# Kernel optimization log

Measured on AMD Instinct MI355X. Metric: run time of the kernel, lower is better.

The kernel has to match this reference:

```python
import jax, jax.numpy as jnp
import numpy as np

S = 3072       # packed sequence length
DIM = 1280     # hidden dim
H = 16         # num heads
HD = DIM // H  # head dim = 80
NEG = -1e9     # additive mask value for cross-segment entries


def setup_inputs() -> dict:
    key = jax.random.key(0)
    ks = jax.random.split(key, 6)
    x = jax.random.normal(ks[0], (S, DIM), jnp.float32)
    # rope angle table [S, HD//2]
    rotary_pos_emb = jax.random.uniform(ks[1], (S, HD // 2), jnp.float32, 0.0, 2.0 * np.pi)
    # 4 equal image segments packed together
    cu_seqlens = jnp.array([0, 768, 1536, 2304, 3072], jnp.int32)
    w_qkv = jax.random.normal(ks[2], (3 * DIM, DIM), jnp.float32) * 0.02
    b_qkv = jax.random.normal(ks[3], (3 * DIM,), jnp.float32) * 0.02
    w_proj = jax.random.normal(ks[4], (DIM, DIM), jnp.float32) * 0.02
    b_proj = jax.random.normal(ks[5], (DIM,), jnp.float32) * 0.02
    return {"x": x, "cu_seqlens": cu_seqlens, "rotary_pos_emb": rotary_pos_emb,
            "w_qkv": w_qkv, "b_qkv": b_qkv, "w_proj": w_proj, "b_proj": b_proj}


def _rope(t, cos, sin):
    # t: [S, H, HD]; cos/sin: [S, 1, HD]
    t1, t2 = jnp.split(t, 2, axis=-1)
    rot = jnp.concatenate([-t2, t1], axis=-1)
    return t * cos + rot * sin


def reference(x, cu_seqlens, rotary_pos_emb, w_qkv, b_qkv, w_proj, b_proj):
    s, d = x.shape
    qkv = (x @ w_qkv.T + b_qkv).reshape(s, 3, H, HD)
    q, k, v = qkv[:, 0], qkv[:, 1], qkv[:, 2]  # each [S, H, HD]

    # NeoX-style rope with tiled (repeated) freqs, computed in fp32
    cos = jnp.cos(rotary_pos_emb)
    sin = jnp.sin(rotary_pos_emb)
    cos = jnp.concatenate([cos, cos], axis=-1)[:, None, :]  # [S,1,HD]
    sin = jnp.concatenate([sin, sin], axis=-1)[:, None, :]
    q = _rope(q.astype(jnp.float32), cos, sin).astype(x.dtype)
    k = _rope(k.astype(jnp.float32), cos, sin).astype(x.dtype)

    # block-diagonal varlen mask from cu_seqlens: segment id per position
    seg = jnp.searchsorted(cu_seqlens, jnp.arange(s), side='right') - 1  # [S]
    mask = jnp.where(seg[:, None] == seg[None, :], 0.0, NEG).astype(x.dtype)  # [S,S]

    scale = 1.0 / np.sqrt(HD).astype(np.float32)
    scores = jnp.einsum('qhd,khd->hqk', q, k) * scale + mask[None]  # [H,S,S]
    attn = jax.nn.softmax(scores, axis=-1)
    out = jnp.einsum('hqk,khd->qhd', attn, v).reshape(s, d)  # [S, DIM]
    return out @ w_proj.T + b_proj
```

## Files before the change

kernel.cpp:

```cpp
#include <hip/hip_runtime.h>


typedef __bf16 bf16;
typedef __bf16 bf16x4 __attribute__((ext_vector_type(4)));
typedef __bf16 bf16x8 __attribute__((ext_vector_type(8)));
typedef float f32x4 __attribute__((ext_vector_type(4)));

constexpr int S = 3072;
constexpr int DIM = 1280;
constexpr int H = 16;
constexpr int HD = 80;
constexpr int DP = 96;
constexpr int NQKV = 3 * DIM;

constexpr float QSCALE = 1.4426950408889634f / 8.94427190999916f;

__device__ __forceinline__ void gload_lds16(const void* g, void* l) {
  __builtin_amdgcn_global_load_lds(
      (const __attribute__((address_space(1))) void*)g,
      (__attribute__((address_space(3))) void*)l, 16, 0, 0);
}

constexpr long CN1 = (long)S * DIM;
constexpr long CN2 = (long)NQKV * DIM;

__global__ __launch_bounds__(256) void cvt3(
    const float* __restrict__ x, const float* __restrict__ wq,
    const float* __restrict__ wp, bf16* __restrict__ xo,
    bf16* __restrict__ wqo, bf16* __restrict__ wpo) {
  long i = ((long)blockIdx.x * 256 + threadIdx.x) * 4;
  const float* s;
  bf16* d;
  if (i < CN1) { s = x + i; d = xo + i; }
  else if (i < CN1 + CN2) { s = wq + (i - CN1); d = wqo + (i - CN1); }
  else { s = wp + (i - CN1 - CN2); d = wpo + (i - CN1 - CN2); }
  float4 v = *(const float4*)s;
  bf16x4 o = {(bf16)v.x, (bf16)v.y, (bf16)v.z, (bf16)v.w};
  *(bf16x4*)d = o;
}

template <bool OUT_BF16>
__global__ __launch_bounds__(512, 2) void gemm256(
    const bf16* __restrict__ A, const bf16* __restrict__ B,
    const float* __restrict__ bias, void* __restrict__ Cout, int M, int N,
    int K) {
  extern __shared__ char lds[];
  const int tid = threadIdx.x;
  const int w = tid >> 6, lane = tid & 63;
  const int r15 = lane & 15, b4 = lane >> 4;
  const int wr = w >> 2, wc = w & 3;
  const int nwg = gridDim.x * gridDim.y;
  const int orig = blockIdx.y * gridDim.x + blockIdx.x;
  const int xcd = orig % 8, loc = orig / 8;
  const int qq = nwg / 8, rq = nwg % 8;
  const int swzid =
      (xcd < rq ? xcd * (qq + 1) : rq * (qq + 1) + (xcd - rq) * qq) + loc;
  const int n0 = (swzid % gridDim.x) * 256, m0 = (swzid / gridDim.x) * 256;
  int aRow[2], aCol[2];
#pragma unroll
  for (int i = 0; i < 2; i++) {
    int lin = (w * 2 + i) * 1024 + lane * 16;
    int logi = lin ^ (((lin >> 7) & 7) << 4);
    aRow[i] = logi >> 6;
    aCol[i] = (logi & 63) >> 1;
  }
  const int NT = K / 32;
  auto stage = [&](int kt) {
    char* sa = lds + (kt & 3) * 32768;
    char* sb = sa + 16384;
    const int kb = kt * 32;
#pragma unroll
    for (int i = 0; i < 2; i++) {
      const int lin = (w * 2 + i) * 1024 + lane * 16;
      gload_lds16(A + (size_t)(m0 + aRow[i]) * K + kb + aCol[i], sa + lin);
      gload_lds16(B + (size_t)(n0 + aRow[i]) * K + kb + aCol[i], sb + lin);
    }
  };
  f32x4 acc[8][4] = {};
  stage(0); stage(1); stage(2);
  asm volatile("s_waitcnt vmcnt(8)" ::: "memory");
  __builtin_amdgcn_s_barrier();
  for (int kt = 0; kt < NT; ++kt) {
    const char* As = lds + (kt & 3) * 32768;
    const char* Bs = As + 16384;
    if (kt + 3 < NT) stage(kt + 3);
    bf16x8 af[8], bfr[4];
#pragma unroll
    for (int i = 0; i < 8; i++) {
      int a = (wr * 128 + i * 16 + r15) * 64 + b4 * 16;
      a ^= ((a >> 7) & 7) << 4;
      af[i] = *(const bf16x8*)(As + a);
    }
#pragma unroll
    for (int j = 0; j < 4; j++) {
      int a = (wc * 64 + j * 16 + r15) * 64 + b4 * 16;
      a ^= ((a >> 7) & 7) << 4;
      bfr[j] = *(const bf16x8*)(Bs + a);
    }
    __builtin_amdgcn_s_setprio(1);
#pragma unroll
    for (int i = 0; i < 8; i++)
#pragma unroll
      for (int j = 0; j < 4; j++)
        acc[i][j] = __builtin_amdgcn_mfma_f32_16x16x32_bf16(af[i], bfr[j],
                                                            acc[i][j], 0, 0, 0);
    __builtin_amdgcn_s_setprio(0);
    const int rem = NT - 2 - kt;
    if (rem >= 2)      asm volatile("s_waitcnt vmcnt(8)" ::: "memory");
    else if (rem == 1) asm volatile("s_waitcnt vmcnt(4)" ::: "memory");
    else if (rem == 0) asm volatile("s_waitcnt vmcnt(0)" ::: "memory");
    else               asm volatile("" ::: "memory");
    __builtin_amdgcn_s_barrier();
  }
#pragma unroll
  for (int j = 0; j < 4; j++) {
    const int n = n0 + wc * 64 + j * 16 + r15;
    const float bv = bias[n];
#pragma unroll
    for (int i = 0; i < 8; i++) {
      const int mr = m0 + wr * 128 + i * 16 + b4 * 4;
#pragma unroll
      for (int r = 0; r < 4; r++) {
        float v = acc[i][j][r] + bv;
        if (OUT_BF16)
          ((bf16*)Cout)[(size_t)(mr + r) * N + n] = (bf16)v;
        else
          ((float*)Cout)[(size_t)(mr + r) * N + n] = v;
      }
    }
  }
}

template <bool OUT_BF16>
__global__ __launch_bounds__(256) void gemm_bt(
    const bf16* __restrict__ A, const bf16* __restrict__ B,
    const float* __restrict__ bias, void* __restrict__ Cout, int M, int N,
    int K) {
  __shared__ bf16 Al[2][128 * 32];
  __shared__ bf16 Bl[2][128 * 32];
  const int tid = threadIdx.x;
  const int w = tid >> 6, lane = tid & 63;
  const int r15 = lane & 15, b4 = lane >> 4;
  const int nwg = gridDim.x * gridDim.y;
  const int orig = blockIdx.y * gridDim.x + blockIdx.x;
  const int swzid = (orig & 7) * (nwg >> 3) + (orig >> 3);
  const int bx = swzid % gridDim.x, by = swzid / gridDim.x;
  const int m0 = by * 128, n0 = bx * 128;
  const int wm = (w >> 1) * 64, wn = (w & 1) * 64;
  f32x4 acc[4][4] = {};
  const int row0 = tid >> 2, ko0 = (tid & 3) * 8;
  const bf16* Ar0 = A + (size_t)(m0 + row0) * K + ko0;
  const bf16* Ar1 = A + (size_t)(m0 + row0 + 64) * K + ko0;
  const bf16* Br0 = B + (size_t)(n0 + row0) * K + ko0;
  const bf16* Br1 = B + (size_t)(n0 + row0 + 64) * K + ko0;

  auto stage = [&](int buf, int k0) {
    char* la = (char*)Al[buf] + w * 1024;
    char* lb = (char*)Bl[buf] + w * 1024;
    gload_lds16(Ar0 + k0, la);
    gload_lds16(Ar1 + k0, la + 4096);
    gload_lds16(Br0 + k0, lb);
    gload_lds16(Br1 + k0, lb + 4096);
  };

  stage(0, 0);
  int cur = 0;
  for (int k0 = 0; k0 < K; k0 += 32) {
    __syncthreads();
    if (k0 + 32 < K) stage(cur ^ 1, k0 + 32);
    bf16x8 af[4], bfr[4];
#pragma unroll
    for (int i = 0; i < 4; i++) {
      af[i] = *(const bf16x8*)((const char*)Al[cur] + (wm + i * 16 + r15) * 64 + b4 * 16);
      bfr[i] = *(const bf16x8*)((const char*)Bl[cur] + (wn + i * 16 + r15) * 64 + b4 * 16);
    }
#pragma unroll
    for (int i = 0; i < 4; i++)
#pragma unroll
      for (int j = 0; j < 4; j++)
        acc[i][j] = __builtin_amdgcn_mfma_f32_16x16x32_bf16(af[i], bfr[j], acc[i][j], 0, 0, 0);
    cur ^= 1;
  }
#pragma unroll
  for (int j = 0; j < 4; j++) {
    const int n = n0 + wn + j * 16 + r15;
    const float bv = bias[n];
#pragma unroll
    for (int i = 0; i < 4; i++) {
      const int mr = m0 + wm + i * 16 + b4 * 4;
#pragma unroll
      for (int r = 0; r < 4; r++) {
        float v = acc[i][j][r] + bv;
        if (OUT_BF16)
          ((bf16*)Cout)[(size_t)(mr + r) * N + n] = (bf16)v;
        else
          ((float*)Cout)[(size_t)(mr + r) * N + n] = v;
      }
    }
  }
}

__global__ __launch_bounds__(256) void rope_scatter(
    const bf16* __restrict__ qkv, const float* __restrict__ rp,
    bf16* __restrict__ Qo, bf16* __restrict__ Ko, bf16* __restrict__ VTo) {
  __shared__ bf16 vl[80][72];
  const int h = blockIdx.x / 48, st = blockIdx.x % 48;
  const int tid = threadIdx.x;
#pragma unroll
  for (int c = 0; c < 3; c++) {
    int ch = c * 256 + tid;
    if (ch < 640) {
      int row = ch / 10, ck = ch % 10;
      int s = st * 64 + row;
      bf16x8 v = *(const bf16x8*)(qkv + (size_t)s * NQKV + 2 * DIM + h * HD + ck * 8);
#pragma unroll
      for (int e = 0; e < 8; e++) vl[ck * 8 + e][row] = v[e];
    }
  }
#pragma unroll
  for (int c = 0; c < 3; c++) {
    int ch = c * 256 + tid;
    if (ch < 640) {
      int row = ch / 10, t10 = ch % 10;
      int which = t10 >= 5 ? 1 : 0, cp = t10 % 5;
      int s = st * 64 + row;
      const bf16* src = qkv + (size_t)s * NQKV + which * DIM + h * HD;
      bf16x8 lo = *(const bf16x8*)(src + cp * 8);
      bf16x8 hi = *(const bf16x8*)(src + 40 + cp * 8);
      const float* rr = rp + (size_t)s * 40 + cp * 8;
      float4 a0 = *(const float4*)rr;
      float4 a1 = *(const float4*)(rr + 4);
      float ang[8] = {a0.x, a0.y, a0.z, a0.w, a1.x, a1.y, a1.z, a1.w};
      const float sc = which ? 1.0f : QSCALE;
      bf16x8 olo, ohi;
#pragma unroll
      for (int e = 0; e < 8; e++) {
        float sn, cs;
        __sincosf(ang[e], &sn, &cs);
        float t1 = (float)lo[e], t2 = (float)hi[e];
        olo[e] = (bf16)((t1 * cs - t2 * sn) * sc);
        ohi[e] = (bf16)((t2 * cs + t1 * sn) * sc);
      }
      bf16* dst = (which ? Ko : Qo) + ((size_t)h * S + s) * DP;
      *(bf16x8*)(dst + cp * 8) = olo;
      *(bf16x8*)(dst + 40 + cp * 8) = ohi;
    }
  }
  {
    int row = tid >> 2, slot = tid & 3;
    int s = st * 64 + row;
    bf16* dst = ((slot >> 1) ? Ko : Qo) + ((size_t)h * S + s) * DP + 80 + (slot & 1) * 8;
    bf16x8 z = {};
    *(bf16x8*)dst = z;
  }
  __syncthreads();
#pragma unroll
  for (int c = 0; c < 3; c++) {
    int ch = c * 256 + tid;
    if (ch < 640) {
      int d = ch >> 3, slot = ch & 7;
      *(bf16x8*)(VTo + (size_t)(h * HD + d) * S + st * 64 + slot * 8) =
          *(const bf16x8*)(&vl[d][slot * 8]);
    }
  }
}

__global__ __launch_bounds__(256) void attn_kern(
    const bf16* __restrict__ Qg, const bf16* __restrict__ Kg,
    const bf16* __restrict__ Vg, const int* __restrict__ cu, int nseg,
    bf16* __restrict__ Out) {
  __shared__ bf16 Kl[2][64 * 128];
  __shared__ bf16 Vl[2][80 * 64];
  __shared__ bf16 Pl[4][16 * 64];
  const int tid = threadIdx.x, w = tid >> 6, lane = tid & 63;
  const int r15 = lane & 15, b4 = lane >> 4;
  const int nwg = gridDim.x;
  const int orig = blockIdx.x;
  const int swzb = (orig & 7) * (nwg >> 3) + (orig >> 3);
  const int h = swzb / 48, qt = swzb % 48;
  const int q = qt * 64 + w * 16 + r15;
  int sq = 0, eq = S, lo = 0, hi = S;
  {
    const int qlo = qt * 64, qhi = qt * 64 + 63;
#pragma unroll
    for (int i = 0; i < 8; i++) {
      if (i >= nseg) break;
      int a = cu[i], b = cu[i + 1];
      if (q >= a && q < b) { sq = a; eq = b; }
      if (qlo >= a && qlo < b) lo = a;
      if (qhi >= a && qhi < b) hi = b;
    }
  }
  const int swz = (r15 & 7) << 4;
  bf16x8 qf[3];
  {
    const bf16* qrow = Qg + ((size_t)h * S + q) * DP + b4 * 8;
#pragma unroll
    for (int c = 0; c < 3; c++) qf[c] = *(const bf16x8*)(qrow + c * 32);
  }
  f32x4 o[5] = {};
  float m = -1e30f, l = 0.f;
  const bf16* Kbase = Kg + (size_t)h * S * DP;
  const bf16* Vbase = Vg + (size_t)h * HD * S;

  int krow[3], kslot[3], vd[3], vslot[3];
#pragma unroll
  for (int c = 0; c < 3; c++) {
    int ch = c * 256 + tid;
    krow[c] = ch / 12; kslot[c] = ch % 12;
    vd[c] = ch >> 3;   vslot[c] = ch & 7;
  }
  bf16x8 kreg[3], vreg[3];

  auto load_stage = [&](int k0) {
#pragma unroll
    for (int c = 0; c < 3; c++)
      kreg[c] = *(const bf16x8*)(Kbase + (size_t)(k0 + krow[c]) * DP + kslot[c] * 8);
#pragma unroll
    for (int c = 0; c < 3; c++)
      if (c < 2 || tid < 128)
        vreg[c] = *(const bf16x8*)(Vbase + (size_t)vd[c] * S + k0 + vslot[c] * 8);
  };
  auto write_stage = [&](int buf) {
#pragma unroll
    for (int c = 0; c < 3; c++)
      *(bf16x8*)((char*)Kl[buf] +
                 ((krow[c] * 256 + kslot[c] * 16) ^ ((krow[c] & 7) << 4))) = kreg[c];
#pragma unroll
    for (int c = 0; c < 3; c++)
      if (c < 2 || tid < 128)
        *(bf16x8*)((char*)Vl[buf] +
                   ((vd[c] * 128 + vslot[c] * 16) ^ ((vd[c] & 7) << 4))) = vreg[c];
  };

  const int k0start = lo & ~63;
  load_stage(k0start);
  write_stage(0);
  __syncthreads();
  int cur = 0;
  for (int k0 = k0start; k0 < hi; k0 += 64) {
    const bool more = (k0 + 64 < hi);
    if (more) load_stage(k0 + 64);
    f32x4 st[4] = {};
    __builtin_amdgcn_s_setprio(1);
#pragma unroll
    for (int g = 0; g < 4; g++)
#pragma unroll
      for (int c = 0; c < 3; c++) {
        bf16x8 kf = *(const bf16x8*)((const char*)Kl[cur] +
                                     (((g * 16 + r15) * 256 + c * 64 + b4 * 16) ^ swz));
        st[g] = __builtin_amdgcn_mfma_f32_16x16x32_bf16(kf, qf[c], st[g], 0, 0, 0);
      }
    __builtin_amdgcn_s_setprio(0);
    float sv[16];
    float tm = -3e38f;
    if (k0 >= sq && k0 + 63 < eq) {
#pragma unroll
      for (int g = 0; g < 4; g++)
#pragma unroll
        for (int r = 0; r < 4; r++) {
          sv[g * 4 + r] = st[g][r];
          tm = fmaxf(tm, st[g][r]);
        }
    } else {
#pragma unroll
      for (int g = 0; g < 4; g++)
#pragma unroll
        for (int r = 0; r < 4; r++) {
          int key = k0 + g * 16 + b4 * 4 + r;
          float sc = (key >= sq && key < eq) ? st[g][r] : -1e30f;
          sv[g * 4 + r] = sc;
          tm = fmaxf(tm, sc);
        }
    }
    tm = fmaxf(tm, __shfl_xor(tm, 16));
    tm = fmaxf(tm, __shfl_xor(tm, 32));
    if (!__all(tm <= m + 8.f)) {
      const float mn = fmaxf(m, tm);
      const float alpha = __builtin_amdgcn_exp2f(m - mn);
#pragma unroll
      for (int dg = 0; dg < 5; dg++) o[dg] *= alpha;
      l *= alpha;
      m = mn;
    }
    float rs = 0.f;
#pragma unroll
    for (int g = 0; g < 4; g++) {
      bf16x4 pp;
#pragma unroll
      for (int r = 0; r < 4; r++) {
        float p = __builtin_amdgcn_exp2f(sv[g * 4 + r] - m);
        rs += p;
        pp[r] = (bf16)p;
      }
      *(bf16x4*)((char*)Pl[w] + ((r15 * 128 + g * 32 + b4 * 8) ^ swz)) = pp;
    }
    rs += __shfl_xor(rs, 16);
    rs += __shfl_xor(rs, 32);
    l += rs;
    __builtin_amdgcn_s_setprio(1);
#pragma unroll
    for (int dg = 0; dg < 5; dg++)
#pragma unroll
      for (int c = 0; c < 2; c++) {
        bf16x8 vf = *(const bf16x8*)((const char*)Vl[cur] +
                                     (((dg * 16 + r15) * 128 + c * 64 + b4 * 16) ^ swz));
        bf16x8 pf = *(const bf16x8*)((const char*)Pl[w] +
                                     ((r15 * 128 + c * 64 + b4 * 16) ^ swz));
        o[dg] = __builtin_amdgcn_mfma_f32_16x16x32_bf16(vf, pf, o[dg], 0, 0, 0);
      }
    __builtin_amdgcn_s_setprio(0);
    if (more) write_stage(cur ^ 1);
    __syncthreads();
    cur ^= 1;
  }
  const float inv = 1.f / l;
  bf16* orow = Out + (size_t)q * DIM + h * HD + b4 * 4;
#pragma unroll
  for (int dg = 0; dg < 5; dg++) {
    bf16x4 ov = {(bf16)(o[dg][0] * inv), (bf16)(o[dg][1] * inv),
                 (bf16)(o[dg][2] * inv), (bf16)(o[dg][3] * inv)};
    *(bf16x4*)(orow + dg * 16) = ov;
  }
}

extern "C" void kernel_launch(void* const* d_in, const int* in_sizes, int n_in,
                              void* d_out, int out_size, void* d_ws,
                              size_t ws_size, hipStream_t stream) {
  const float* x = (const float*)d_in[0];
  const int* cu = (const int*)d_in[1];
  const float* rope = (const float*)d_in[2];
  const float* w_qkv = (const float*)d_in[3];
  const float* b_qkv = (const float*)d_in[4];
  const float* w_proj = (const float*)d_in[5];
  const float* b_proj = (const float*)d_in[6];
  const int nseg = in_sizes[1] - 1;

  bf16* x16 = (bf16*)d_ws;
  bf16* wq16 = x16 + (size_t)S * DIM;
  bf16* wp16 = wq16 + (size_t)NQKV * DIM;
  bf16* qkv16 = wp16 + (size_t)DIM * DIM;
  bf16* Qb = qkv16 + (size_t)S * NQKV;
  bf16* Kb = Qb + (size_t)H * S * DP;
  bf16* VTb = Kb + (size_t)H * S * DP;
  bf16* attn16 = VTb + (size_t)H * HD * S;

  cvt3<<<10240, 256, 0, stream>>>(x, w_qkv, w_proj, x16, wq16, wp16);
  gemm256<true><<<dim3(NQKV / 256, S / 256), 512, 131072, stream>>>(
      x16, wq16, b_qkv, qkv16, S, NQKV, DIM);
  rope_scatter<<<H * 48, 256, 0, stream>>>(qkv16, rope, Qb, Kb, VTb);
  attn_kern<<<H * 48, 256, 0, stream>>>(Qb, Kb, VTb, cu, nseg, attn16);
  gemm_bt<false><<<dim3(DIM / 128, S / 128), 256, 0, stream>>>(
      attn16, wp16, b_proj, d_out, S, DIM, DIM);
}
```

Baseline: 132.5 us.

## Split GEMM k-step into two half-phases interleaving A/B prefetch with MFMA

```diff
diff --git a/kernel.cpp b/kernel.cpp
--- a/kernel.cpp
+++ b/kernel.cpp
@@ -56,40 +56,43 @@
   const int swzid =
       (xcd < rq ? xcd * (qq + 1) : rq * (qq + 1) + (xcd - rq) * qq) + loc;
   const int n0 = (swzid % gridDim.x) * 256, m0 = (swzid / gridDim.x) * 256;
-  int aRow[2], aCol[2];
+  const bf16* aSrc[2];
+  const bf16* bSrc[2];
+  int linv[2];
 #pragma unroll
   for (int i = 0; i < 2; i++) {
-    int lin = (w * 2 + i) * 1024 + lane * 16;
-    int logi = lin ^ (((lin >> 7) & 7) << 4);
-    aRow[i] = logi >> 6;
-    aCol[i] = (logi & 63) >> 1;
+    const int lin = tid * 16 + i * 8192;
+    linv[i] = lin;
+    const int logi = lin ^ (((lin >> 7) & 7) << 4);
+    const int row = logi >> 6, col = (logi & 63) >> 1;
+    aSrc[i] = A + (size_t)(m0 + row) * K + col;
+    bSrc[i] = B + (size_t)(n0 + row) * K + col;
   }
   const int NT = K / 32;
-  auto stage = [&](int kt) {
-    char* sa = lds + (kt & 3) * 32768;
-    char* sb = sa + 16384;
-    const int kb = kt * 32;
-#pragma unroll
-    for (int i = 0; i < 2; i++) {
-      const int lin = (w * 2 + i) * 1024 + lane * 16;
-      gload_lds16(A + (size_t)(m0 + aRow[i]) * K + kb + aCol[i], sa + lin);
-      gload_lds16(B + (size_t)(n0 + aRow[i]) * K + kb + aCol[i], sb + lin);
-    }
+  auto stageA = [&](int kt) {
+    char* s = lds + (kt & 3) * 32768;
+#pragma unroll
+    for (int i = 0; i < 2; i++) gload_lds16(aSrc[i] + kt * 32, s + linv[i]);
+  };
+  auto stageB = [&](int kt) {
+    char* s = lds + (kt & 3) * 32768 + 16384;
+#pragma unroll
+    for (int i = 0; i < 2; i++) gload_lds16(bSrc[i] + kt * 32, s + linv[i]);
   };
   f32x4 acc[8][4] = {};
-  stage(0); stage(1); stage(2);
+  stageA(0); stageB(0); stageA(1); stageB(1); stageA(2); stageB(2);
   asm volatile("s_waitcnt vmcnt(8)" ::: "memory");
   __builtin_amdgcn_s_barrier();
   for (int kt = 0; kt < NT; ++kt) {
     const char* As = lds + (kt & 3) * 32768;
     const char* Bs = As + 16384;
-    if (kt + 3 < NT) stage(kt + 3);
-    bf16x8 af[8], bfr[4];
-#pragma unroll
-    for (int i = 0; i < 8; i++) {
+    const bool pf = (kt + 3 < NT);
+    bf16x8 afr[4], bfr[4];
+#pragma unroll
+    for (int i = 0; i < 4; i++) {
       int a = (wr * 128 + i * 16 + r15) * 64 + b4 * 16;
       a ^= ((a >> 7) & 7) << 4;
-      af[i] = *(const bf16x8*)(As + a);
+      afr[i] = *(const bf16x8*)(As + a);
     }
 #pragma unroll
     for (int j = 0; j < 4; j++) {
@@ -97,13 +100,35 @@
       a ^= ((a >> 7) & 7) << 4;
       bfr[j] = *(const bf16x8*)(Bs + a);
     }
+    if (pf) stageA(kt + 3);
+    asm volatile("" ::: "memory");
+    __builtin_amdgcn_s_barrier();
     __builtin_amdgcn_s_setprio(1);
 #pragma unroll
-    for (int i = 0; i < 8; i++)
+    for (int i = 0; i < 4; i++)
 #pragma unroll
       for (int j = 0; j < 4; j++)
-        acc[i][j] = __builtin_amdgcn_mfma_f32_16x16x32_bf16(af[i], bfr[j],
+        acc[i][j] = __builtin_amdgcn_mfma_f32_16x16x32_bf16(afr[i], bfr[j],
                                                             acc[i][j], 0, 0, 0);
+    __builtin_amdgcn_s_setprio(0);
+    asm volatile("" ::: "memory");
+    __builtin_amdgcn_s_barrier();
+#pragma unroll
+    for (int i = 0; i < 4; i++) {
+      int a = (wr * 128 + 64 + i * 16 + r15) * 64 + b4 * 16;
+      a ^= ((a >> 7) & 7) << 4;
+      afr[i] = *(const bf16x8*)(As + a);
+    }
+    if (pf) stageB(kt + 3);
+    asm volatile("" ::: "memory");
+    __builtin_amdgcn_s_barrier();
+    __builtin_amdgcn_s_setprio(1);
+#pragma unroll
+    for (int i = 0; i < 4; i++)
+#pragma unroll
+      for (int j = 0; j < 4; j++)
+        acc[4 + i][j] = __builtin_amdgcn_mfma_f32_16x16x32_bf16(
+            afr[i], bfr[j], acc[4 + i][j], 0, 0, 0);
     __builtin_amdgcn_s_setprio(0);
     const int rem = NT - 2 - kt;
     if (rem >= 2)      asm volatile("s_waitcnt vmcnt(8)" ::: "memory");
```

After: 134.1 us. About the same (+1.3%).
